# Performance work log

Measured on AMD Instinct MI355X. Metric: run time of the kernel, lower is better.

## Reference

```python
import jax, jax.numpy as jnp
import numpy as np

D_X = 256
D_Z = 64
D = D_X + D_Z  # total_d
H = 16         # num_hidden
B = 1024
NEG_SLOPE = 0.01  # torch LeakyReLU default
LOG_2PI = float(np.log(2.0 * np.pi))


def _fixed_mask():
    fm = jnp.ones((D, D), dtype=jnp.float32)
    idx = jnp.arange(D_Z, D)
    fm = fm.at[idx, idx].set(0.0)          # zero diag for observed block
    fm = fm.at[:, :D_Z].set(0.0)           # zero columns into latents
    idz = jnp.arange(D_Z)
    fm = fm.at[idz, idz].set(1.0)          # keep latent self-links
    return fm


def setup_inputs() -> dict:
    key = jax.random.key(0)
    ks = jax.random.split(key, 11)
    eps = 1e-6
    return {
        "x": jax.random.normal(ks[0], (B, D_X), dtype=jnp.float32),
        "z": jax.random.normal(ks[1], (B, D_Z), dtype=jnp.float32),
        "u": jax.random.uniform(ks[2], (B, D, D), dtype=jnp.float32, minval=eps, maxval=1.0 - eps),
        "mask_param": jax.random.normal(ks[3], (D, D), dtype=jnp.float32) + 1.0,
        "W0": jax.random.normal(ks[4], (D, D, H), dtype=jnp.float32) * (1.0 / np.sqrt(D)),
        "b0": jax.random.normal(ks[5], (D, H), dtype=jnp.float32) * 0.1,
        "W1": jax.random.normal(ks[6], (D, H, H), dtype=jnp.float32) * (1.0 / np.sqrt(H)),
        "b1": jax.random.normal(ks[7], (D, H), dtype=jnp.float32) * 0.1,
        "W2": jax.random.normal(ks[8], (D, H), dtype=jnp.float32) * (1.0 / np.sqrt(H)),
        "b2": jax.random.normal(ks[9], (D,), dtype=jnp.float32) * 0.1,
        "logvar": jnp.full((1, D), -4.0, dtype=jnp.float32),
    }


def reference(x, z, u, mask_param, W0, b0, W1, b1, W2, b2, logvar):
    # --- Mask.forward: soft gumbel-sigmoid sample, elementwise fixed mask ---
    logistic = jnp.log(u) - jnp.log1p(-u)                 # [b, D, D]
    adj = jax.nn.sigmoid(mask_param[None] + logistic)      # [b, D, D]
    adj = adj * _fixed_mask()[None]

    # --- transition: vectorized over k (the total_d per-variable MLPs) ---
    all_var = jnp.concatenate((z, x), axis=1)               # [b, D]
    # mask[:, :, k] * all_var  ->  masked[b, k, j] = adj[b, j, k] * all_var[b, j]
    masked = jnp.swapaxes(adj, 1, 2) * all_var[:, None, :]  # [b, D_k, D_j]

    h = jnp.einsum("bkj,kjh->bkh", masked, W0) + b0[None]   # [b, D, H]
    h = jax.nn.leaky_relu(h, NEG_SLOPE)
    h = jnp.einsum("bkh,khg->bkg", h, W1) + b1[None]        # [b, D, H]
    h = jax.nn.leaky_relu(h, NEG_SLOPE)
    mu = jnp.einsum("bkh,kh->bk", h, W2) + b2[None]         # [b, D]

    std = jnp.exp(0.5 * logvar)                              # [1, D]

    # --- Gaussian log_prob of cat(z, x), sum over features, mean over batch ---
    diff = (all_var - mu) / std
    logp = -0.5 * diff * diff - jnp.log(std) - 0.5 * LOG_2PI  # [b, D]
    recons = jnp.mean(jnp.sum(logp, axis=1))
    return recons, mu, std
```

## Files before the change

### kernel.cpp

```cpp
#include <hip/hip_runtime.h>
#include <math.h>

#define D_TOT 320
#define D_ZL  64
#define D_XO  256
#define NH    16
#define NB_B  1024
#define NEG   0.01f
#define HALF_LOG2PI 0.9189385332046727f

#define W0P_OFF  0
#define W0P_SZ   (5*320*64*16)
#define W1P_OFF  (W0P_OFF + W0P_SZ)
#define W1P_SZ   (5*256*64)
#define W2P_OFF  (W1P_OFF + W1P_SZ)
#define W2P_SZ   (5*16*64)
#define CM_OFF   (W2P_OFF + W2P_SZ)
#define CM_SZ    (320*320)
#define PART_OFF (CM_OFF + CM_SZ)
#define PART_SZ  1024
#define PRE_TOTAL (CM_SZ + W1P_SZ + W2P_SZ + D_TOT + PART_SZ)

__global__ __launch_bounds__(256) void pre_small(
    const float* __restrict__ mp, const float* __restrict__ W1,
    const float* __restrict__ W2, const float* __restrict__ logvar,
    float* __restrict__ ws, float* __restrict__ out) {
  int i = blockIdx.x * 256 + threadIdx.x;
  if (i < CM_SZ) {
    int j = i / 320, k = i - j * 320;
    bool fm = (k < D_ZL) ? (j == k) : (j != k);
    ws[CM_OFF + i] = fm ? expf(-mp[i]) : INFINITY;
  }
  int i1 = i - CM_SZ;
  if (i1 >= 0 && i1 < W1P_SZ) {
    int lane = i1 & 63; int r = i1 >> 6;
    int tile = r >> 8;  int hg = r & 255;
    ws[W1P_OFF + i1] = W1[(tile * 64 + lane) * 256 + hg];
  }
  int i2 = i1 - W1P_SZ;
  if (i2 >= 0 && i2 < W2P_SZ) {
    int lane = i2 & 63; int r = i2 >> 6;
    int tile = r >> 4;  int h = r & 15;
    ws[W2P_OFF + i2] = W2[(tile * 64 + lane) * 16 + h];
  }
  int i3 = i2 - W2P_SZ;
  if (i3 >= 0 && i3 < D_TOT) {
    out[1 + NB_B * D_TOT + i3] = expf(0.5f * logvar[i3]);
  }
  int i4 = i3 - D_TOT;
  if (i4 >= 0 && i4 < PART_SZ) ws[PART_OFF + i4] = 0.0f;
}

__global__ __launch_bounds__(256) void repack_w0(
    const float* __restrict__ W0, float* __restrict__ ws) {
  int i = blockIdx.x * 256 + threadIdx.x;
  int h = i & 15;    int r = i >> 4;
  int lane = r & 63; int jj = r >> 6;
  int tile = jj / 320; int j = jj - tile * 320;
  ws[W0P_OFF + i] = W0[((tile * 64 + lane) * 320 + j) * 16 + h];
}

__global__ __launch_bounds__(256) void main_k(
    const float* __restrict__ x, const float* __restrict__ z,
    const float* __restrict__ u, const float* __restrict__ bias0,
    const float* __restrict__ bias1, const float* __restrict__ bias2,
    const float* __restrict__ logvar, float* __restrict__ ws,
    float* __restrict__ out) {
  int swz  = (blockIdx.x & 7) * 80 + (blockIdx.x >> 3);
  int tile = swz >> 7;
  int bblk = swz & 127;
  int tid  = threadIdx.x;
  int wave = tid >> 6, lane = tid & 63;
  int k     = tile * 64 + lane;
  int bbase = bblk * 8;
  int bA    = bbase + wave * 2;
  int bB    = bA + 1;

  __shared__ float av[8][320];
  for (int t = tid; t < 8 * 320; t += 256) {
    int bb = t / 320, jj = t - (t / 320) * 320;
    av[bb][jj] = (jj < D_ZL) ? z[(bbase + bb) * D_ZL + jj]
                             : x[(bbase + bb) * D_XO + (jj - D_ZL)];
  }
  __syncthreads();

  float acc0[16], acc1[16];
#pragma unroll
  for (int h = 0; h < NH; ++h) {
    float bv = bias0[k * NH + h];
    acc0[h] = bv; acc1[h] = bv;
  }

  const float* w0p = ws + W0P_OFF + tile * (320 * 64 * 16) + lane * 16;
  const float* cmp = ws + CM_OFF + k;
  const float* uA  = u + bA * (320 * 320) + k;
  const float* uB  = u + bB * (320 * 320) + k;
  const float* avA = &av[wave * 2][0];
  const float* avB = &av[wave * 2 + 1][0];

#pragma unroll 2
  for (int j = 0; j < 320; ++j) {
    float c  = cmp[j * 320];
    float u0 = uA[j * 320];
    float u1 = uB[j * 320];
    float r0 = __builtin_amdgcn_rcpf(fmaf(c, 1.0f - u0, u0));
    float r1 = __builtin_amdgcn_rcpf(fmaf(c, 1.0f - u1, u1));
    float m0 = u0 * r0 * avA[j];
    float m1 = u1 * r1 * avB[j];
    const float4* wr = (const float4*)(w0p + j * 1024);
    float4 wv0 = wr[0], wv1 = wr[1], wv2 = wr[2], wv3 = wr[3];
    acc0[ 0]=fmaf(m0,wv0.x,acc0[ 0]); acc0[ 1]=fmaf(m0,wv0.y,acc0[ 1]);
    acc0[ 2]=fmaf(m0,wv0.z,acc0[ 2]); acc0[ 3]=fmaf(m0,wv0.w,acc0[ 3]);
    acc0[ 4]=fmaf(m0,wv1.x,acc0[ 4]); acc0[ 5]=fmaf(m0,wv1.y,acc0[ 5]);
    acc0[ 6]=fmaf(m0,wv1.z,acc0[ 6]); acc0[ 7]=fmaf(m0,wv1.w,acc0[ 7]);
    acc0[ 8]=fmaf(m0,wv2.x,acc0[ 8]); acc0[ 9]=fmaf(m0,wv2.y,acc0[ 9]);
    acc0[10]=fmaf(m0,wv2.z,acc0[10]); acc0[11]=fmaf(m0,wv2.w,acc0[11]);
    acc0[12]=fmaf(m0,wv3.x,acc0[12]); acc0[13]=fmaf(m0,wv3.y,acc0[13]);
    acc0[14]=fmaf(m0,wv3.z,acc0[14]); acc0[15]=fmaf(m0,wv3.w,acc0[15]);
    acc1[ 0]=fmaf(m1,wv0.x,acc1[ 0]); acc1[ 1]=fmaf(m1,wv0.y,acc1[ 1]);
    acc1[ 2]=fmaf(m1,wv0.z,acc1[ 2]); acc1[ 3]=fmaf(m1,wv0.w,acc1[ 3]);
    acc1[ 4]=fmaf(m1,wv1.x,acc1[ 4]); acc1[ 5]=fmaf(m1,wv1.y,acc1[ 5]);
    acc1[ 6]=fmaf(m1,wv1.z,acc1[ 6]); acc1[ 7]=fmaf(m1,wv1.w,acc1[ 7]);
    acc1[ 8]=fmaf(m1,wv2.x,acc1[ 8]); acc1[ 9]=fmaf(m1,wv2.y,acc1[ 9]);
    acc1[10]=fmaf(m1,wv2.z,acc1[10]); acc1[11]=fmaf(m1,wv2.w,acc1[11]);
    acc1[12]=fmaf(m1,wv3.x,acc1[12]); acc1[13]=fmaf(m1,wv3.y,acc1[13]);
    acc1[14]=fmaf(m1,wv3.z,acc1[14]); acc1[15]=fmaf(m1,wv3.w,acc1[15]);
  }

  const float* w1p = ws + W1P_OFF + tile * (256 * 64) + lane;
  const float* w2p = ws + W2P_OFF + tile * (16 * 64) + lane;
  float h1a[16], h1b[16];
#pragma unroll
  for (int g = 0; g < NH; ++g) {
    float bv = bias1[k * NH + g];
    h1a[g] = bv; h1b[g] = bv;
  }
#pragma unroll
  for (int h = 0; h < NH; ++h) {
    float v0 = acc0[h]; v0 = v0 > 0.0f ? v0 : NEG * v0;
    float v1 = acc1[h]; v1 = v1 > 0.0f ? v1 : NEG * v1;
#pragma unroll
    for (int g = 0; g < NH; ++g) {
      float wv = w1p[(h * 16 + g) * 64];
      h1a[g] = fmaf(v0, wv, h1a[g]);
      h1b[g] = fmaf(v1, wv, h1b[g]);
    }
  }
  float muA = bias2[k], muB = bias2[k];
#pragma unroll
  for (int h = 0; h < NH; ++h) {
    float v0 = h1a[h]; v0 = v0 > 0.0f ? v0 : NEG * v0;
    float v1 = h1b[h]; v1 = v1 > 0.0f ? v1 : NEG * v1;
    float wv = w2p[h * 64];
    muA = fmaf(v0, wv, muA);
    muB = fmaf(v1, wv, muB);
  }
  out[1 + bA * 320 + k] = muA;
  out[1 + bB * 320 + k] = muB;

  float lv   = logvar[k];
  float rstd = expf(-0.5f * lv);
  float dA = (avA[k] - muA) * rstd;
  float dB = (avB[k] - muB) * rstd;
  float base = -0.5f * lv - HALF_LOG2PI;
  float lpA = fmaf(-0.5f * dA, dA, base);
  float lpB = fmaf(-0.5f * dB, dB, base);
#pragma unroll
  for (int off = 32; off > 0; off >>= 1) {
    lpA += __shfl_xor(lpA, off);
    lpB += __shfl_xor(lpB, off);
  }
  if (lane == 0) {
    atomicAdd(&ws[PART_OFF + bA], lpA);
    atomicAdd(&ws[PART_OFF + bB], lpB);
  }
}

__global__ __launch_bounds__(256) void finalize(
    const float* __restrict__ ws, float* __restrict__ out) {
  int tid = threadIdx.x;
  float v = 0.0f;
  for (int i = tid; i < PART_SZ; i += 256) v += ws[PART_OFF + i];
#pragma unroll
  for (int off = 32; off > 0; off >>= 1) v += __shfl_xor(v, off);
  __shared__ float s[4];
  if ((tid & 63) == 0) s[tid >> 6] = v;
  __syncthreads();
  if (tid == 0) out[0] = (s[0] + s[1] + s[2] + s[3]) * (1.0f / (float)NB_B);
}

extern "C" void kernel_launch(void* const* d_in, const int* in_sizes, int n_in,
                              void* d_out, int out_size, void* d_ws, size_t ws_size,
                              hipStream_t stream) {
  const float* x  = (const float*)d_in[0];
  const float* z  = (const float*)d_in[1];
  const float* u  = (const float*)d_in[2];
  const float* mp = (const float*)d_in[3];
  const float* W0 = (const float*)d_in[4];
  const float* b0 = (const float*)d_in[5];
  const float* W1 = (const float*)d_in[6];
  const float* b1 = (const float*)d_in[7];
  const float* W2 = (const float*)d_in[8];
  const float* b2 = (const float*)d_in[9];
  const float* lv = (const float*)d_in[10];
  float* out = (float*)d_out;
  float* ws  = (float*)d_ws;

  hipLaunchKernelGGL(pre_small, dim3((PRE_TOTAL + 255) / 256), dim3(256), 0, stream,
                     mp, W1, W2, lv, ws, out);
  hipLaunchKernelGGL(repack_w0, dim3(W0P_SZ / 256), dim3(256), 0, stream, W0, ws);
  hipLaunchKernelGGL(main_k, dim3(640), dim3(256), 0, stream,
                     x, z, u, b0, b1, b2, lv, ws, out);
  hipLaunchKernelGGL(finalize, dim3(1), dim3(256), 0, stream, ws, out);
}
```

Before: 810.5 us.

## Software-pipeline u loads in groups and merge prep kernels into one launch

The main j-loop now loads u values in groups of 8 into double-buffered registers, prefetching the next group while computing the current one. This is meant to hide the latency of the strided u reads, which dominate memory traffic. The W0 repack and the small preprocessing kernel are merged into a single launch to remove one kernel launch. The cost is higher register pressure from the extra buffers, which may reduce occupancy.

Result: slower. 953.5 us (+17.6%).

```diff
diff --git a/kernel.cpp b/kernel.cpp
--- a/kernel.cpp
+++ b/kernel.cpp
@@ -8,6 +8,7 @@
 #define NB_B  1024
 #define NEG   0.01f
 #define HALF_LOG2PI 0.9189385332046727f
+#define GROUP 8
 
 #define W0P_OFF  0
 #define W0P_SZ   (5*320*64*16)
@@ -19,19 +20,29 @@
 #define CM_SZ    (320*320)
 #define PART_OFF (CM_OFF + CM_SZ)
 #define PART_SZ  1024
-#define PRE_TOTAL (CM_SZ + W1P_SZ + W2P_SZ + D_TOT + PART_SZ)
-
-__global__ __launch_bounds__(256) void pre_small(
-    const float* __restrict__ mp, const float* __restrict__ W1,
-    const float* __restrict__ W2, const float* __restrict__ logvar,
-    float* __restrict__ ws, float* __restrict__ out) {
+#define SMALL_TOTAL (CM_SZ + W1P_SZ + W2P_SZ + D_TOT + PART_SZ)
+#define PREP_TOTAL  (W0P_SZ + SMALL_TOTAL)
+
+__global__ __launch_bounds__(256) void prep(
+    const float* __restrict__ W0, const float* __restrict__ mp,
+    const float* __restrict__ W1, const float* __restrict__ W2,
+    const float* __restrict__ logvar, float* __restrict__ ws,
+    float* __restrict__ out) {
   int i = blockIdx.x * 256 + threadIdx.x;
-  if (i < CM_SZ) {
-    int j = i / 320, k = i - j * 320;
+  if (i < W0P_SZ) {
+    int h = i & 15;    int r = i >> 4;
+    int lane = r & 63; int jj = r >> 6;
+    int tile = jj / 320; int j = jj - tile * 320;
+    ws[W0P_OFF + i] = W0[((tile * 64 + lane) * 320 + j) * 16 + h];
+    return;
+  }
+  int q = i - W0P_SZ;
+  if (q < CM_SZ) {
+    int j = q / 320, k = q - j * 320;
     bool fm = (k < D_ZL) ? (j == k) : (j != k);
-    ws[CM_OFF + i] = fm ? expf(-mp[i]) : INFINITY;
-  }
-  int i1 = i - CM_SZ;
+    ws[CM_OFF + q] = fm ? expf(-mp[q]) : INFINITY;
+  }
+  int i1 = q - CM_SZ;
   if (i1 >= 0 && i1 < W1P_SZ) {
     int lane = i1 & 63; int r = i1 >> 6;
     int tile = r >> 8;  int hg = r & 255;
@@ -51,63 +62,34 @@
   if (i4 >= 0 && i4 < PART_SZ) ws[PART_OFF + i4] = 0.0f;
 }
 
-__global__ __launch_bounds__(256) void repack_w0(
-    const float* __restrict__ W0, float* __restrict__ ws) {
-  int i = blockIdx.x * 256 + threadIdx.x;
-  int h = i & 15;    int r = i >> 4;
-  int lane = r & 63; int jj = r >> 6;
-  int tile = jj / 320; int j = jj - tile * 320;
-  ws[W0P_OFF + i] = W0[((tile * 64 + lane) * 320 + j) * 16 + h];
-}
-
-__global__ __launch_bounds__(256) void main_k(
-    const float* __restrict__ x, const float* __restrict__ z,
-    const float* __restrict__ u, const float* __restrict__ bias0,
-    const float* __restrict__ bias1, const float* __restrict__ bias2,
-    const float* __restrict__ logvar, float* __restrict__ ws,
-    float* __restrict__ out) {
-  int swz  = (blockIdx.x & 7) * 80 + (blockIdx.x >> 3);
-  int tile = swz >> 7;
-  int bblk = swz & 127;
-  int tid  = threadIdx.x;
-  int wave = tid >> 6, lane = tid & 63;
-  int k     = tile * 64 + lane;
-  int bbase = bblk * 8;
-  int bA    = bbase + wave * 2;
-  int bB    = bA + 1;
-
-  __shared__ float av[8][320];
-  for (int t = tid; t < 8 * 320; t += 256) {
-    int bb = t / 320, jj = t - (t / 320) * 320;
-    av[bb][jj] = (jj < D_ZL) ? z[(bbase + bb) * D_ZL + jj]
-                             : x[(bbase + bb) * D_XO + (jj - D_ZL)];
-  }
-  __syncthreads();
-
-  float acc0[16], acc1[16];
-#pragma unroll
-  for (int h = 0; h < NH; ++h) {
-    float bv = bias0[k * NH + h];
-    acc0[h] = bv; acc1[h] = bv;
-  }
-
-  const float* w0p = ws + W0P_OFF + tile * (320 * 64 * 16) + lane * 16;
-  const float* cmp = ws + CM_OFF + k;
-  const float* uA  = u + bA * (320 * 320) + k;
-  const float* uB  = u + bB * (320 * 320) + k;
-  const float* avA = &av[wave * 2][0];
-  const float* avB = &av[wave * 2 + 1][0];
-
-#pragma unroll 2
-  for (int j = 0; j < 320; ++j) {
-    float c  = cmp[j * 320];
-    float u0 = uA[j * 320];
-    float u1 = uB[j * 320];
-    float r0 = __builtin_amdgcn_rcpf(fmaf(c, 1.0f - u0, u0));
-    float r1 = __builtin_amdgcn_rcpf(fmaf(c, 1.0f - u1, u1));
-    float m0 = u0 * r0 * avA[j];
-    float m1 = u1 * r1 * avB[j];
-    const float4* wr = (const float4*)(w0p + j * 1024);
+__device__ __forceinline__ void load_u(const float* __restrict__ uA,
+                                       const float* __restrict__ uB, int j0,
+                                       float (&gu0)[GROUP], float (&gu1)[GROUP]) {
+#pragma unroll
+  for (int t = 0; t < GROUP; ++t) {
+    gu0[t] = uA[(j0 + t) * 320];
+    gu1[t] = uB[(j0 + t) * 320];
+  }
+}
+
+__device__ __forceinline__ void comp_g(const float* __restrict__ cmp,
+                                       const float* avA, const float* avB,
+                                       const float* __restrict__ w0p, int j0,
+                                       const float (&gu0)[GROUP], const float (&gu1)[GROUP],
+                                       float (&acc0)[16], float (&acc1)[16]) {
+  float cb[GROUP], aA[GROUP], aB[GROUP];
+#pragma unroll
+  for (int t = 0; t < GROUP; ++t) cb[t] = cmp[(j0 + t) * 320];
+#pragma unroll
+  for (int t = 0; t < GROUP; ++t) { aA[t] = avA[j0 + t]; aB[t] = avB[j0 + t]; }
+#pragma unroll
+  for (int t = 0; t < GROUP; ++t) {
+    float u0 = gu0[t], u1 = gu1[t], cc = cb[t];
+    float r0 = __builtin_amdgcn_rcpf(fmaf(cc, 1.0f - u0, u0));
+    float r1 = __builtin_amdgcn_rcpf(fmaf(cc, 1.0f - u1, u1));
+    float m0 = u0 * r0 * aA[t];
+    float m1 = u1 * r1 * aB[t];
+    const float4* wr = (const float4*)(w0p + (size_t)(j0 + t) * 1024);
     float4 wv0 = wr[0], wv1 = wr[1], wv2 = wr[2], wv3 = wr[3];
     acc0[ 0]=fmaf(m0,wv0.x,acc0[ 0]); acc0[ 1]=fmaf(m0,wv0.y,acc0[ 1]);
     acc0[ 2]=fmaf(m0,wv0.z,acc0[ 2]); acc0[ 3]=fmaf(m0,wv0.w,acc0[ 3]);
@@ -126,6 +108,58 @@
     acc1[12]=fmaf(m1,wv3.x,acc1[12]); acc1[13]=fmaf(m1,wv3.y,acc1[13]);
     acc1[14]=fmaf(m1,wv3.z,acc1[14]); acc1[15]=fmaf(m1,wv3.w,acc1[15]);
   }
+}
+
+__global__ __launch_bounds__(256) void main_k(
+    const float* __restrict__ x, const float* __restrict__ z,
+    const float* __restrict__ u, const float* __restrict__ bias0,
+    const float* __restrict__ bias1, const float* __restrict__ bias2,
+    const float* __restrict__ logvar, float* __restrict__ ws,
+    float* __restrict__ out) {
+  int swz  = (blockIdx.x & 7) * 80 + (blockIdx.x >> 3);
+  int tile = swz >> 7;
+  int bblk = swz & 127;
+  int tid  = threadIdx.x;
+  int wave = tid >> 6, lane = tid & 63;
+  int k     = tile * 64 + lane;
+  int bbase = bblk * 8;
+  int bA    = bbase + wave * 2;
+  int bB    = bA + 1;
+
+  __shared__ float av[8][320];
+  for (int t = tid; t < 8 * 320; t += 256) {
+    int bb = t / 320, jj = t - (t / 320) * 320;
+    av[bb][jj] = (jj < D_ZL) ? z[(bbase + bb) * D_ZL + jj]
+                             : x[(bbase + bb) * D_XO + (jj - D_ZL)];
+  }
+  __syncthreads();
+
+  float acc0[16], acc1[16];
+#pragma unroll
+  for (int h = 0; h < NH; ++h) {
+    float bv = bias0[k * NH + h];
+    acc0[h] = bv; acc1[h] = bv;
+  }
+
+  const float* w0p = ws + W0P_OFF + tile * (320 * 64 * 16) + lane * 16;
+  const float* cmp = ws + CM_OFF + k;
+  const float* uA  = u + (size_t)bA * (320 * 320) + k;
+  const float* uB  = u + (size_t)bB * (320 * 320) + k;
+  const float* avA = &av[wave * 2][0];
+  const float* avB = &av[wave * 2 + 1][0];
+
+  float buA0[GROUP], buB0[GROUP], buA1[GROUP], buB1[GROUP];
+  load_u(uA, uB, 0, buA0, buB0);
+#pragma unroll 1
+  for (int g = 0; g + 2 < 40; g += 2) {
+    load_u(uA, uB, (g + 1) * GROUP, buA1, buB1);
+    comp_g(cmp, avA, avB, w0p, g * GROUP, buA0, buB0, acc0, acc1);
+    load_u(uA, uB, (g + 2) * GROUP, buA0, buB0);
+    comp_g(cmp, avA, avB, w0p, (g + 1) * GROUP, buA1, buB1, acc0, acc1);
+  }
+  load_u(uA, uB, 39 * GROUP, buA1, buB1);
+  comp_g(cmp, avA, avB, w0p, 38 * GROUP, buA0, buB0, acc0, acc1);
+  comp_g(cmp, avA, avB, w0p, 39 * GROUP, buA1, buB1, acc0, acc1);
 
   const float* w1p = ws + W1P_OFF + tile * (256 * 64) + lane;
   const float* w2p = ws + W2P_OFF + tile * (16 * 64) + lane;
@@ -206,9 +240,8 @@
   float* out = (float*)d_out;
   float* ws  = (float*)d_ws;
 
-  hipLaunchKernelGGL(pre_small, dim3((PRE_TOTAL + 255) / 256), dim3(256), 0, stream,
-                     mp, W1, W2, lv, ws, out);
-  hipLaunchKernelGGL(repack_w0, dim3(W0P_SZ / 256), dim3(256), 0, stream, W0, ws);
+  hipLaunchKernelGGL(prep, dim3((PREP_TOTAL + 255) / 256), dim3(256), 0, stream,
+                     W0, mp, W1, W2, lv, ws, out);
   hipLaunchKernelGGL(main_k, dim3(640), dim3(256), 0, stream,
                      x, z, u, b0, b1, b2, lv, ws, out);
   hipLaunchKernelGGL(finalize, dim3(1), dim3(256), 0, stream, ws, out);
```
